# Optimization experiments

Hardware: AMD Instinct MI355X
Metric: run time of the kernel (lower is better)

The kernel has to match this reference:

```python
import jax, jax.numpy as jnp
import numpy as np

B, N_C, N_T, D, DF = 16, 2048, 1024, 2, 2
K, E_OBS = 16, 4
H, DH = 4, 16
F = H * DH  # 64-dim node features (embed_all output)


def setup_inputs() -> dict:
    key = jax.random.key(0)
    ks = jax.random.split(key, 16)
    r = lambda i, shape: jax.random.normal(ks[i], shape, jnp.float32) * 0.05
    d_in = E_OBS + D + DF  # obs(4) + s(2) + f(2) = 8
    return dict(
        s_ctx=jax.random.normal(ks[0], (B, N_C, D), jnp.float32),
        f_ctx=jax.random.normal(ks[1], (B, N_C, DF), jnp.float32),
        s_test=jax.random.normal(ks[2], (B, N_T, D), jnp.float32),
        emb_obs=r(3, (2, E_OBS)),
        W1=r(4, (d_in, 256)), b1=jnp.zeros((256,), jnp.float32),
        W2=r(5, (256, 128)), b2=jnp.zeros((128,), jnp.float32),
        W3=r(6, (128, F)), b3=jnp.zeros((F,), jnp.float32),
        ln_g=jnp.ones((F,), jnp.float32), ln_b=jnp.zeros((F,), jnp.float32),
        Wg=r(7, (F, F)),
        a_src=r(8, (H, DH)), a_dst=r(9, (H, DH)),
        We=r(10, (D, H)), be=jnp.zeros((H,), jnp.float32),
        H1=r(11, (F, 256)), c1=jnp.zeros((256,), jnp.float32),
        H2=r(12, (256, 64)), c2=jnp.zeros((64,), jnp.float32),
        H3=r(13, (64, 2)), c3=jnp.zeros((2,), jnp.float32),
    )


def _knn(q, ctx, k):
    # q [B,Nq,D], ctx [B,Nc,D] -> neighbor indices [B,Nq,K] and displacement edge feats [B,Nq,K,D]
    d2 = (jnp.sum(q * q, -1)[:, :, None] + jnp.sum(ctx * ctx, -1)[:, None, :]
          - 2.0 * jnp.einsum('bqd,bcd->bqc', q, ctx))
    _, idx = jax.lax.top_k(-d2, k)
    nb = jax.vmap(lambda c, i: c[i])(ctx, idx)  # gather neighbor coords per batch
    return idx, q[:, :, None, :] - nb


def _mlp3(x, W1, b1, W2, b2, W3, b3):
    x = jax.nn.gelu(x @ W1 + b1)
    x = jax.nn.gelu(x @ W2 + b2)
    return x @ W3 + b3


def _ln(x, g, b):
    mu = jnp.mean(x, -1, keepdims=True)
    v = jnp.var(x, -1, keepdims=True)
    return (x - mu) * jax.lax.rsqrt(v + 1e-6) * g + b


def reference(s_ctx, f_ctx, s_test, emb_obs, W1, b1, W2, b2, W3, b3, ln_g, ln_b,
              Wg, a_src, a_dst, We, be, H1, c1, H2, c2, H3, c3):
    # --- build kNN graph (ctx->ctx and ctx->test edges, K per receiver) ---
    s_cc, d_cc = _knn(s_ctx, s_ctx, K)
    s_ct, d_ct = _knn(s_test, s_ctx, K)
    edges = jnp.concatenate([d_cc.reshape(-1, D), d_ct.reshape(-1, D)], axis=0)  # [E, D]
    off = (jnp.arange(B) * N_C)[:, None, None]
    senders = jnp.concatenate([(s_cc + off).reshape(-1), (s_ct + off).reshape(-1)])  # [E]
    # receivers == repeat(arange(N), K): edges are grouped K-per-node in node order.

    # --- node embedding: [obs_embed | s | f] -> MLP -> LayerNorm ---
    ctx_in = jnp.concatenate([jnp.broadcast_to(emb_obs[1], (B, N_C, E_OBS)), s_ctx, f_ctx], -1)
    test_in = jnp.concatenate([jnp.broadcast_to(emb_obs[0], (B, N_T, E_OBS)), s_test,
                               jnp.zeros((B, N_T, DF), s_test.dtype)], -1)
    n_ctx = _ln(_mlp3(ctx_in, W1, b1, W2, b2, W3, b3), ln_g, ln_b)
    n_test = _ln(_mlp3(test_in, W1, b1, W2, b2, W3, b3), ln_g, ln_b)
    nodes = jnp.concatenate([n_ctx.reshape(B * N_C, F), n_test.reshape(B * N_T, F)], 0)
    N = B * (N_C + N_T)

    # --- edge-biased GAT message passing (K incoming edges per node) ---
    xp = (nodes @ Wg).reshape(N, H, DH)
    msg = xp[senders].reshape(N, K, H, DH)  # gather sender features
    sc = (jnp.einsum('nkhd,hd->nkh', msg, a_src)
          + jnp.einsum('nhd,hd->nh', xp, a_dst)[:, None, :])
    sc = jax.nn.leaky_relu(sc, 0.2) + (edges @ We + be).reshape(N, K, H)  # edge bias
    alpha = jax.nn.softmax(sc, axis=1)  # softmax over the K neighbors
    out = jnp.einsum('nkh,nkhd->nhd', alpha, msg).reshape(N, F)
    nodes = nodes + out  # residual

    # --- head on test nodes + diagonal MVN output ---
    n_t = nodes[-B * N_T:].reshape(B, N_T, F)
    o = jax.nn.gelu(n_t @ H1 + c1)
    o = jax.nn.gelu(o @ H2 + c2)
    o = o @ H3 + c3  # [B, N_t, 2]
    mean = o[..., 0:1]
    scale = jax.nn.softplus(o[..., 1:2])
    return jnp.concatenate([mean, scale], -1)
```

## Files before the change

kernel.cpp:

```cpp
#include <hip/hip_runtime.h>
#include <math.h>

#define NB 16
#define NCTX 2048
#define NTEST 1024
#define NCTX_TOT (NB*NCTX)
#define NTEST_TOT (NB*NTEST)
#define NTOT (NCTX_TOT + NTEST_TOT)

typedef _Float16 half8 __attribute__((ext_vector_type(8)));
typedef _Float16 half4 __attribute__((ext_vector_type(4)));
typedef float f32x4 __attribute__((ext_vector_type(4)));

__device__ __forceinline__ float gelu_f(float x) {
  float x3 = x * x * x;
  float y = 0.7978845608028654f * fmaf(0.044715f, x3, x);
  float e = __expf(2.0f * y);
  float th = 1.0f - 2.0f * __builtin_amdgcn_rcpf(e + 1.0f);
  return 0.5f * x * (1.0f + th);
}

__device__ __forceinline__ void fma4(float4& a, float s, float4 w) {
  a.x = fmaf(s, w.x, a.x);
  a.y = fmaf(s, w.y, a.y);
  a.z = fmaf(s, w.z, a.z);
  a.w = fmaf(s, w.w, a.w);
}

__device__ __forceinline__ float4 ldg4(const float* p) {
  return *reinterpret_cast<const float4*>(p);
}

__device__ __forceinline__ unsigned fkey(float f) {
  unsigned u = __float_as_uint(f);
  return (u & 0x80000000u) ? ~u : (u ^ 0x80000000u);
}
__device__ __forceinline__ float unfkey(unsigned k) {
  return (k & 0x80000000u) ? __uint_as_float(k ^ 0x80000000u)
                           : __uint_as_float(~k);
}

__global__ __launch_bounds__(256, 6) void knn_prep_kernel(
    const float* __restrict__ s_ctx, const float* __restrict__ s_test,
    int* __restrict__ senders,
    const float* __restrict__ W1, const float* __restrict__ b1,
    const float* __restrict__ emb,
    const float* __restrict__ W2, const float* __restrict__ W3,
    const float* __restrict__ Wg,
    const float* __restrict__ H1, const float* __restrict__ H2,
    _Float16* __restrict__ W2P, _Float16* __restrict__ W3P,
    _Float16* __restrict__ WgP,
    _Float16* __restrict__ H1P, _Float16* __restrict__ H2P,
    float* __restrict__ ctype)
{
  __shared__ __align__(16) unsigned long long sk[4][128];
  const int blk = blockIdx.x;

  if (blk < 40) {
    const int t = blk*256 + (int)threadIdx.x;
    if (t < 4096) {
      int i = t;
      int j = i >> 9, ks = (i >> 6) & 7, l = i & 63;
      int col = 16*j + (l & 15);
      int k0  = ks*32 + (l >> 4)*8;
      half8 o;
      #pragma unroll
      for (int e = 0; e < 8; ++e) o[e] = (_Float16)W2[(k0 + e)*128 + col];
      *reinterpret_cast<half8*>(&W2P[(size_t)i*8]) = o;
    } else if (t < 5120) {
      int i = t - 4096;
      int j = i >> 8, ks = (i >> 6) & 3, l = i & 63;
      int col = 16*j + (l & 15);
      int k0  = ks*32 + (l >> 4)*8;
      half8 o;
      #pragma unroll
      for (int e = 0; e < 8; ++e) o[e] = (_Float16)W3[(k0 + e)*64 + col];
      *reinterpret_cast<half8*>(&W3P[(size_t)i*8]) = o;
    } else if (t < 5632) {
      int i = t - 5120;
      int j = i >> 7, ks = (i >> 6) & 1, l = i & 63;
      int col = 16*j + (l & 15);
      int k0  = ks*32 + (l >> 4)*8;
      half8 o;
      #pragma unroll
      for (int e = 0; e < 8; ++e) o[e] = (_Float16)Wg[(k0 + e)*64 + col];
      *reinterpret_cast<half8*>(&WgP[(size_t)i*8]) = o;
    } else if (t < 7680) {
      int i = t - 5632;
      int j = i >> 7, ks = (i >> 6) & 1, l = i & 63;
      int col = 16*j + (l & 15);
      int k0  = ks*32 + (l >> 4)*8;
      half8 o;
      #pragma unroll
      for (int e = 0; e < 8; ++e) o[e] = (_Float16)H1[(k0 + e)*256 + col];
      *reinterpret_cast<half8*>(&H1P[(size_t)i*8]) = o;
    } else if (t < 9728) {
      int i = t - 7680;
      int j = i >> 9, ks = (i >> 6) & 7, l = i & 63;
      int col = 16*j + (l & 15);
      int k0  = ks*32 + (l >> 4)*8;
      half8 o;
      #pragma unroll
      for (int e = 0; e < 8; ++e) o[e] = (_Float16)H2[(k0 + e)*64 + col];
      *reinterpret_cast<half8*>(&H2P[(size_t)i*8]) = o;
    } else {
      int i = t - 9728;
      int ty = i >> 8, c = i & 255;
      float acc = b1[c];
      #pragma unroll
      for (int k = 0; k < 4; ++k) acc = fmaf(emb[ty*4 + k], W1[k*256 + c], acc);
      ctype[i] = acc;
    }
    return;
  }

  const int t    = threadIdx.x;
  const int lane = t & 63;
  const int w    = t >> 6;
  const int blk2 = blk - 40;
  const int bb   = blk2 >> 8;
  const int q    = (blk2 & 255) * 4 + w;
  const int trow = bb * NTEST + q;

  const float* cb = s_ctx + (size_t)bb * NCTX * 2;
  const float qx = s_test[(size_t)trow*2];
  const float qy = s_test[(size_t)trow*2 + 1];
  const float qq = __fadd_rn(__fmul_rn(qx,qx), __fmul_rn(qy,qy));

  float d[32];
  float mn = 3.4e38f;
  #pragma unroll
  for (int it = 0; it < 32; ++it) {
    float2 p = *reinterpret_cast<const float2*>(&cb[2*(it*64 + lane)]);
    float ss  = __fadd_rn(__fmul_rn(p.x,p.x), __fmul_rn(p.y,p.y));
    float dot = __fadd_rn(__fmul_rn(qx, p.x), __fmul_rn(qy, p.y));
    float d2  = __fsub_rn(__fadd_rn(qq, ss), __fmul_rn(2.0f, dot));
    d[it] = d2;
    mn = fminf(mn, d2);
  }

  unsigned key = fkey(mn);
  unsigned acc = 0u;
  #pragma unroll
  for (int bit = 31; bit >= 0; --bit) {
    unsigned candv = acc | (1u << bit);
    unsigned long long bal = __ballot(key < candv);
    if (__popcll(bal) < 16) acc = candv;
  }
  const float Tf = unfkey(acc);

  int base = 0;
  #pragma unroll
  for (int it = 0; it < 32; ++it) {
    bool pr = (d[it] <= Tf);
    unsigned long long m = __ballot(pr);
    if (pr) {
      int pos = base + __popcll(m & ((1ULL << lane) - 1ULL));
      if (pos < 128)
        sk[w][pos] = ((unsigned long long)fkey(d[it]) << 32)
                   | (unsigned)(it*64 + lane);
    }
    base += __popcll(m);
  }
  const int S = base;

  if (S <= 32) {
    if (lane >= S && lane < 32) sk[w][lane] = ~0ULL;
    unsigned long long pm = sk[w][lane & 31];
    int r0 = 0;
    #pragma unroll
    for (int j = 0; j < 32; ++j)
      r0 += (int)(sk[w][j] < pm);
    if (lane < S && r0 < 16)
      senders[(size_t)trow*16 + r0] = bb*NCTX + (int)(pm & 0xFFFFFFFFu);
  } else if (S <= 128) {
    unsigned long long p0 = (lane      < S) ? sk[w][lane]      : ~0ULL;
    unsigned long long p1 = (lane + 64 < S) ? sk[w][lane + 64] : ~0ULL;
    int r0 = 0, r1 = 0;
    for (int j = 0; j < S; ++j) {
      unsigned long long kj = sk[w][j];
      r0 += (int)(kj < p0);
      r1 += (int)(kj < p1);
    }
    if (lane < S && r0 < 16)
      senders[(size_t)trow*16 + r0] = bb*NCTX + (int)(p0 & 0xFFFFFFFFu);
    if (lane + 64 < S && r1 < 16)
      senders[(size_t)trow*16 + r1] = bb*NCTX + (int)(p1 & 0xFFFFFFFFu);
  } else {
    if (lane == 0) {
      float dist[16]; int ind[16];
      #pragma unroll
      for (int j=0;j<16;++j){ dist[j]=3.4e38f; ind[j]=0; }
      for (int c = 0; c < NCTX; ++c) {
        float2 p = *reinterpret_cast<const float2*>(&cb[2*c]);
        float ss  = __fadd_rn(__fmul_rn(p.x,p.x), __fmul_rn(p.y,p.y));
        float dot = __fadd_rn(__fmul_rn(qx, p.x), __fmul_rn(qy, p.y));
        float d2  = __fsub_rn(__fadd_rn(qq, ss), __fmul_rn(2.0f, dot));
        if (d2 < dist[15]) {
          float dj = d2; int ij = c;
          #pragma unroll
          for (int j = 0; j < 16; ++j) {
            bool sw = dj < dist[j];
            float td = dist[j]; int ti = ind[j];
            dist[j] = sw ? dj : td;  ind[j] = sw ? ij : ti;
            dj = sw ? td : dj;       ij = sw ? ti : ij;
          }
        }
      }
      for (int j = 0; j < 16; ++j)
        senders[(size_t)trow*16 + j] = bb*NCTX + ind[j];
    }
  }
}

__global__ __launch_bounds__(256, 4) void mlp_kernel(
    const float* __restrict__ s_ctx, const float* __restrict__ f_ctx,
    const float* __restrict__ s_test,
    const float* __restrict__ ctype, const float* __restrict__ W1,
    const _Float16* __restrict__ W2P, const float* __restrict__ b2,
    const _Float16* __restrict__ W3P, const float* __restrict__ b3,
    const float* __restrict__ ln_g, const float* __restrict__ ln_b,
    const _Float16* __restrict__ WgP,
    const float* __restrict__ a_src, const float* __restrict__ a_dst,
    float* __restrict__ nodes, _Float16* __restrict__ xph,
    float* __restrict__ xps, float* __restrict__ xpd)
{
  __shared__ __align__(16) char smem[34816];
  const int t    = threadIdx.x;
  const int lane = t & 63;
  const int w    = t >> 6;
  const int id   = blockIdx.x;
  char* slice = smem + w * 8704;
  _Float16* h1t  = reinterpret_cast<_Float16*>(slice);
  float (*xin)[4] = reinterpret_cast<float(*)[4]>(slice + 8448);
  _Float16* h2   = h1t;
  _Float16* nodh = h1t + 16*136;
  const int cn = lane & 15;
  const int kg = lane >> 4;
  const int m0 = (id*4 + w) * 16;
  const bool is_ctx = (m0 < NCTX_TOT);

  const _Float16* bQ2 = W2P + lane*8;
  const _Float16* bQ3 = W3P + lane*8;
  const _Float16* bQg = WgP + lane*8;

  half8 bb2[8];
  #pragma unroll
  for (int j = 0; j < 8; ++j)
    bb2[j] = *reinterpret_cast<const half8*>(bQ2 + j*4096);

  {
    int r = lane >> 2, c = lane & 3;
    int n = m0 + r;
    float v;
    if (is_ctx) v = (c < 2) ? s_ctx[2*(size_t)n + c] : f_ctx[2*(size_t)n + (c-2)];
    else { int tn = n - NCTX_TOT; v = (c < 2) ? s_test[2*(size_t)tn + c] : 0.f; }
    xin[r][c] = v;
  }

  {
    const int c0 = lane * 4;
    float4 w4 = ldg4(&W1[4*256 + c0]);
    float4 w5 = ldg4(&W1[5*256 + c0]);
    float4 w6 = ldg4(&W1[6*256 + c0]);
    float4 w7 = ldg4(&W1[7*256 + c0]);
    float4 cbv = ldg4(&ctype[(is_ctx ? 256 : 0) + c0]);
    #pragma unroll
    for (int r = 0; r < 16; ++r) {
      float4 xi = *reinterpret_cast<const float4*>(&xin[r][0]);
      float4 a = cbv;
      fma4(a, xi.x, w4); fma4(a, xi.y, w5);
      fma4(a, xi.z, w6); fma4(a, xi.w, w7);
      half4 o = { (_Float16)gelu_f(a.x), (_Float16)gelu_f(a.y),
                  (_Float16)gelu_f(a.z), (_Float16)gelu_f(a.w) };
      *reinterpret_cast<half4*>(&h1t[r*264 + c0]) = o;
    }
  }

  {
    f32x4 acc[8];
    #pragma unroll
    for (int j = 0; j < 8; ++j) {
      float bv = b2[16*j + cn];
      acc[j] = (f32x4){bv, bv, bv, bv};
    }
    const _Float16* aP = h1t + cn*264 + kg*8;
    #pragma unroll
    for (int ks = 0; ks < 8; ++ks) {
      half8 a = *reinterpret_cast<const half8*>(aP + ks*32);
      half8 bn[8];
      if (ks < 7) {
        #pragma unroll
        for (int j = 0; j < 8; ++j)
          bn[j] = *reinterpret_cast<const half8*>(bQ2 + j*4096 + (ks+1)*512);
      }
      #pragma unroll
      for (int j = 0; j < 8; ++j)
        acc[j] = __builtin_amdgcn_mfma_f32_16x16x32_f16(a, bb2[j], acc[j], 0, 0, 0);
      if (ks < 7) {
        #pragma unroll
        for (int j = 0; j < 8; ++j) bb2[j] = bn[j];
      }
    }
    #pragma unroll
    for (int j = 0; j < 8; ++j)
      #pragma unroll
      for (int r = 0; r < 4; ++r) {
        int m = kg*4 + r;
        h2[m*136 + 16*j + cn] = (_Float16)gelu_f(acc[j][r]);
      }
  }

  {
    f32x4 acc[4];
    #pragma unroll
    for (int j = 0; j < 4; ++j) {
      float bv = b3[16*j + cn];
      acc[j] = (f32x4){bv, bv, bv, bv};
    }
    const _Float16* aP = h2 + cn*136 + kg*8;
    half8 bb[4];
    #pragma unroll
    for (int j = 0; j < 4; ++j)
      bb[j] = *reinterpret_cast<const half8*>(bQ3 + j*2048);
    #pragma unroll
    for (int ks = 0; ks < 4; ++ks) {
      half8 a = *reinterpret_cast<const half8*>(aP + ks*32);
      half8 bn[4];
      if (ks < 3) {
        #pragma unroll
        for (int j = 0; j < 4; ++j)
          bn[j] = *reinterpret_cast<const half8*>(bQ3 + j*2048 + (ks+1)*512);
      }
      #pragma unroll
      for (int j = 0; j < 4; ++j)
        acc[j] = __builtin_amdgcn_mfma_f32_16x16x32_f16(a, bb[j], acc[j], 0, 0, 0);
      if (ks < 3) {
        #pragma unroll
        for (int j = 0; j < 4; ++j) bb[j] = bn[j];
      }
    }
    float gv[4], bvv[4];
    #pragma unroll
    for (int j = 0; j < 4; ++j) { gv[j] = ln_g[16*j+cn]; bvv[j] = ln_b[16*j+cn]; }
    const bool is_test = !is_ctx;
    #pragma unroll
    for (int r = 0; r < 4; ++r) {
      float sv = 0.f, sq = 0.f;
      #pragma unroll
      for (int j = 0; j < 4; ++j) {
        float v = acc[j][r];
        sv += v; sq += v*v;
      }
      #pragma unroll
      for (int o = 1; o < 16; o <<= 1) {
        sv += __shfl_xor(sv, o);
        sq += __shfl_xor(sq, o);
      }
      float mean = sv * (1.0f/64.0f);
      float var  = sq * (1.0f/64.0f) - mean*mean;
      float rstd = rsqrtf(var + 1e-6f);
      int m = kg*4 + r;
      #pragma unroll
      for (int j = 0; j < 4; ++j) {
        float v = (acc[j][r] - mean) * rstd * gv[j] + bvv[j];
        nodh[m*72 + 16*j + cn] = (_Float16)v;
        if (is_test)
          nodes[(size_t)(m0 + m)*64 + 16*j + cn] = v;
      }
    }
  }

  {
    f32x4 acc[4];
    #pragma unroll
    for (int j = 0; j < 4; ++j) acc[j] = (f32x4){0.f, 0.f, 0.f, 0.f};
    const _Float16* aP = nodh + cn*72 + kg*8;
    half8 bg0[4], bg1[4];
    #pragma unroll
    for (int j = 0; j < 4; ++j) {
      bg0[j] = *reinterpret_cast<const half8*>(bQg + j*1024);
      bg1[j] = *reinterpret_cast<const half8*>(bQg + j*1024 + 512);
    }
    half8 a0 = *reinterpret_cast<const half8*>(aP);
    half8 a1 = *reinterpret_cast<const half8*>(aP + 32);
    #pragma unroll
    for (int j = 0; j < 4; ++j)
      acc[j] = __builtin_amdgcn_mfma_f32_16x16x32_f16(a0, bg0[j], acc[j], 0, 0, 0);
    #pragma unroll
    for (int j = 0; j < 4; ++j)
      acc[j] = __builtin_amdgcn_mfma_f32_16x16x32_f16(a1, bg1[j], acc[j], 0, 0, 0);
    #pragma unroll
    for (int r = 0; r < 4; ++r) {
      int m = kg*4 + r;
      #pragma unroll
      for (int j = 0; j < 4; ++j)
        xph[(size_t)(m0 + m)*64 + 16*j + cn] = (_Float16)acc[j][r];
    }
    const float* av = is_ctx ? a_src : a_dst;
    float av0 = av[cn], av1 = av[16+cn], av2 = av[32+cn], av3 = av[48+cn];
    #pragma unroll
    for (int r = 0; r < 4; ++r) {
      float p0 = acc[0][r]*av0, p1 = acc[1][r]*av1;
      float p2 = acc[2][r]*av2, p3 = acc[3][r]*av3;
      #pragma unroll
      for (int o = 1; o < 16; o <<= 1) {
        p0 += __shfl_xor(p0, o); p1 += __shfl_xor(p1, o);
        p2 += __shfl_xor(p2, o); p3 += __shfl_xor(p3, o);
      }
      if (cn == 0) {
        int m = kg*4 + r;
        float4 v = make_float4(p0, p1, p2, p3);
        if (is_ctx)
          *reinterpret_cast<float4*>(&xps[(size_t)(m0 + m)*4]) = v;
        else
          *reinterpret_cast<float4*>(&xpd[(size_t)(m0 + m - NCTX_TOT)*4]) = v;
      }
    }
  }
}

__global__ __launch_bounds__(64, 3) void back_kernel(
    const float* __restrict__ s_ctx, const float* __restrict__ s_test,
    const _Float16* __restrict__ xph, const int* __restrict__ senders,
    const float* __restrict__ xps, const float* __restrict__ xpd,
    const float* __restrict__ We, const float* __restrict__ be,
    const float* __restrict__ nodes,
    const _Float16* __restrict__ H1P, const float* __restrict__ c1,
    const _Float16* __restrict__ H2P, const float* __restrict__ c2,
    const float* __restrict__ H3, const float* __restrict__ c3,
    float* __restrict__ outp)
{
  __shared__ __align__(16) _Float16 xinh[16*72];
  __shared__ __align__(16) _Float16 h1[16*264];
  const int lane = threadIdx.x;
  const int cn   = lane & 15;
  const int kg   = lane >> 4;
  const int bid  = blockIdx.x;
  const int L    = (bid & 7)*256 + (bid >> 3);
  const int row0 = L * 8;

  #pragma unroll
  for (int rr = 8; rr < 16; ++rr) xinh[rr*72 + lane] = (_Float16)0.f;

  {
    const int h  = kg;
    const int kk = cn;
    const int hb = lane & 48;
    const float we0 = We[h], we1 = We[4+h], beh = be[h];
    for (int rr = 0; rr < 8; ++rr) {
      const int trow = row0 + rr;
      int s = senders[(size_t)trow*16 + kk];
      s = (s < 0) ? 0 : ((s >= NCTX_TOT) ? NCTX_TOT - 1 : s);
      float pre = xps[(size_t)s*4 + h] + xpd[(size_t)trow*4 + h];
      float lr  = pre >= 0.f ? pre : 0.2f * pre;
      const float qx = s_test[(size_t)trow*2];
      const float qy = s_test[(size_t)trow*2 + 1];
      float ex = qx - s_ctx[(size_t)s*2];
      float ey = qy - s_ctx[(size_t)s*2 + 1];
      float sc = lr + fmaf(ex, we0, fmaf(ey, we1, beh));
      float mx = sc;
      #pragma unroll
      for (int o = 1; o < 16; o <<= 1) mx = fmaxf(mx, __shfl_xor(mx, o));
      float e = __expf(sc - mx);
      float sum = e;
      #pragma unroll
      for (int o = 1; o < 16; o <<= 1) sum += __shfl_xor(sum, o);
      float alpha = e / sum;
      float outv = 0.f;
      #pragma unroll
      for (int k = 0; k < 16; ++k) {
        int   sk = __shfl(s, k);
        float al = __shfl(alpha, hb + k);
        outv = fmaf(al, (float)xph[(size_t)sk*64 + lane], outv);
      }
      float xv = nodes[(size_t)(NCTX_TOT + trow)*64 + lane] + outv;
      xinh[rr*72 + lane] = (_Float16)xv;
    }
  }

  {
    const _Float16* aP  = xinh + cn*72 + kg*8;
    const _Float16* bQ1 = H1P + lane*8;
    half8 a0 = *reinterpret_cast<const half8*>(aP);
    half8 a1 = *reinterpret_cast<const half8*>(aP + 32);
    #pragma unroll
    for (int g = 0; g < 2; ++g) {
      f32x4 acc[8];
      #pragma unroll
      for (int j = 0; j < 8; ++j) {
        float bv = c1[16*(g*8 + j) + cn];
        acc[j] = (f32x4){bv, bv, bv, bv};
      }
      half8 b0[8], b1[8];
      #pragma unroll
      for (int j = 0; j < 8; ++j) {
        b0[j] = *reinterpret_cast<const half8*>(bQ1 + ((g*8 + j)*2 + 0)*512);
        b1[j] = *reinterpret_cast<const half8*>(bQ1 + ((g*8 + j)*2 + 1)*512);
      }
      #pragma unroll
      for (int j = 0; j < 8; ++j)
        acc[j] = __builtin_amdgcn_mfma_f32_16x16x32_f16(a0, b0[j], acc[j], 0, 0, 0);
      #pragma unroll
      for (int j = 0; j < 8; ++j)
        acc[j] = __builtin_amdgcn_mfma_f32_16x16x32_f16(a1, b1[j], acc[j], 0, 0, 0);
      #pragma unroll
      for (int j = 0; j < 8; ++j)
        #pragma unroll
        for (int r = 0; r < 4; ++r)
          h1[(kg*4 + r)*264 + 16*(g*8 + j) + cn] = (_Float16)gelu_f(acc[j][r]);
    }
  }

  {
    f32x4 acc[4];
    #pragma unroll
    for (int j = 0; j < 4; ++j) {
      float bv = c2[16*j + cn];
      acc[j] = (f32x4){bv, bv, bv, bv};
    }
    const _Float16* aP  = h1 + cn*264 + kg*8;
    const _Float16* bQ2 = H2P + lane*8;
    half8 bb[4];
    #pragma unroll
    for (int j = 0; j < 4; ++j)
      bb[j] = *reinterpret_cast<const half8*>(bQ2 + j*4096);
    #pragma unroll
    for (int ks = 0; ks < 8; ++ks) {
      half8 a = *reinterpret_cast<const half8*>(aP + ks*32);
      half8 bn[4];
      if (ks < 7) {
        #pragma unroll
        for (int j = 0; j < 4; ++j)
          bn[j] = *reinterpret_cast<const half8*>(bQ2 + j*4096 + (ks+1)*512);
      }
      #pragma unroll
      for (int j = 0; j < 4; ++j)
        acc[j] = __builtin_amdgcn_mfma_f32_16x16x32_f16(a, bb[j], acc[j], 0, 0, 0);
      if (ks < 7) {
        #pragma unroll
        for (int j = 0; j < 4; ++j) bb[j] = bn[j];
      }
    }
    float h30[4], h31[4];
    #pragma unroll
    for (int j = 0; j < 4; ++j) {
      h30[j] = H3[(16*j + cn)*2 + 0];
      h31[j] = H3[(16*j + cn)*2 + 1];
    }
    const float c30 = c3[0], c31 = c3[1];
    #pragma unroll
    for (int r = 0; r < 4; ++r) {
      float p0 = 0.f, p1 = 0.f;
      #pragma unroll
      for (int j = 0; j < 4; ++j) {
        float g = gelu_f(acc[j][r]);
        p0 = fmaf(g, h30[j], p0);
        p1 = fmaf(g, h31[j], p1);
      }
      #pragma unroll
      for (int o = 1; o < 16; o <<= 1) {
        p0 += __shfl_xor(p0, o);
        p1 += __shfl_xor(p1, o);
      }
      if (cn == 0 && kg < 2) {
        int row = row0 + kg*4 + r;
        float m = p0 + c30;
        float sa = p1 + c31;
        float sv = fmaxf(sa, 0.f) + log1pf(__expf(-fabsf(sa)));
        outp[(size_t)row*2 + 0] = m;
        outp[(size_t)row*2 + 1] = sv;
      }
    }
  }
}

extern "C" void kernel_launch(void* const* d_in, const int* in_sizes, int n_in,
                              void* d_out, int out_size, void* d_ws, size_t ws_size,
                              hipStream_t stream) {
  const float* s_ctx  = (const float*)d_in[0];
  const float* f_ctx  = (const float*)d_in[1];
  const float* s_test = (const float*)d_in[2];
  const float* emb    = (const float*)d_in[3];
  const float* W1 = (const float*)d_in[4];
  const float* b1 = (const float*)d_in[5];
  const float* W2 = (const float*)d_in[6];
  const float* b2 = (const float*)d_in[7];
  const float* W3 = (const float*)d_in[8];
  const float* b3 = (const float*)d_in[9];
  const float* ln_g = (const float*)d_in[10];
  const float* ln_b = (const float*)d_in[11];
  const float* Wg = (const float*)d_in[12];
  const float* a_src = (const float*)d_in[13];
  const float* a_dst = (const float*)d_in[14];
  const float* We = (const float*)d_in[15];
  const float* be = (const float*)d_in[16];
  const float* H1 = (const float*)d_in[17];
  const float* c1 = (const float*)d_in[18];
  const float* H2 = (const float*)d_in[19];
  const float* c2 = (const float*)d_in[20];
  const float* H3 = (const float*)d_in[21];
  const float* c3 = (const float*)d_in[22];

  float* nodes   = (float*)d_ws;
  _Float16* xph  = (_Float16*)(nodes + (size_t)NTOT*64);
  int*   senders = (int*)(xph + (size_t)NTOT*64);
  _Float16* W2P  = (_Float16*)(senders + (size_t)NTEST_TOT*16);
  _Float16* W3P  = W2P + 32768;
  _Float16* WgP  = W3P + 8192;
  _Float16* H1P  = WgP + 4096;
  _Float16* H2P  = H1P + 16384;
  float*   ctype = (float*)(H2P + 16384);
  float*   xps   = ctype + 512;
  float*   xpd   = xps + (size_t)NCTX_TOT*4;
  float* outp    = (float*)d_out;

  hipLaunchKernelGGL(knn_prep_kernel, dim3(4136), dim3(256), 0, stream,
                     s_ctx, s_test, senders,
                     W1, b1, emb, W2, W3, Wg, H1, H2,
                     W2P, W3P, WgP, H1P, H2P, ctype);
  hipLaunchKernelGGL(mlp_kernel, dim3(768), dim3(256), 0, stream,
                     s_ctx, f_ctx, s_test, ctype, W1,
                     W2P, b2, W3P, b3, ln_g, ln_b, WgP,
                     a_src, a_dst, nodes, xph, xps, xpd);
  hipLaunchKernelGGL(back_kernel, dim3(2048), dim3(64), 0, stream,
                     s_ctx, s_test, xph, senders, xps, xpd, We, be,
                     nodes, H1P, c1, H2P, c2, H3, c3, outp);
}
```

Baseline: 71.71 us.

## Process two kNN queries per wavefront using half-wave lanes

The kNN selection in knn_prep_kernel now assigns two test queries to each 64-lane wavefront, each handled by 32 lanes that scan 64 context points apiece. The radix-select threshold search and the ballot-based compaction run both halves at once by splitting ballot masks, which halves the grid size and the number of ballot/bit-search iterations per query. In exchange each lane keeps twice as many distances in registers (the launch-bounds occupancy hint is lowered to match), and the rank-sort fallback loops to the larger of the two halves' candidate counts.

```diff
diff --git a/kernel.cpp b/kernel.cpp
--- a/kernel.cpp
+++ b/kernel.cpp
@@ -40,7 +40,7 @@
                            : __uint_as_float(~k);
 }
 
-__global__ __launch_bounds__(256, 6) void knn_prep_kernel(
+__global__ __launch_bounds__(256, 4) void knn_prep_kernel(
     const float* __restrict__ s_ctx, const float* __restrict__ s_test,
     int* __restrict__ senders,
     const float* __restrict__ W1, const float* __restrict__ b1,
@@ -53,7 +53,7 @@
     _Float16* __restrict__ H1P, _Float16* __restrict__ H2P,
     float* __restrict__ ctype)
 {
-  __shared__ __align__(16) unsigned long long sk[4][128];
+  __shared__ __align__(16) unsigned long long sk[4][2][128];
   const int blk = blockIdx.x;
 
   if (blk < 40) {
@@ -117,9 +117,12 @@
   const int t    = threadIdx.x;
   const int lane = t & 63;
   const int w    = t >> 6;
+  const int half = lane >> 5;
+  const int hl   = lane & 31;
   const int blk2 = blk - 40;
-  const int bb   = blk2 >> 8;
-  const int q    = (blk2 & 255) * 4 + w;
+  const int qid  = blk2*8 + (w << 1) + half;
+  const int bb   = qid >> 10;
+  const int q    = qid & 1023;
   const int trow = bb * NTEST + q;
 
   const float* cb = s_ctx + (size_t)bb * NCTX * 2;
@@ -127,11 +130,11 @@
   const float qy = s_test[(size_t)trow*2 + 1];
   const float qq = __fadd_rn(__fmul_rn(qx,qx), __fmul_rn(qy,qy));
 
-  float d[32];
+  float d[64];
   float mn = 3.4e38f;
   #pragma unroll
-  for (int it = 0; it < 32; ++it) {
-    float2 p = *reinterpret_cast<const float2*>(&cb[2*(it*64 + lane)]);
+  for (int it = 0; it < 64; ++it) {
+    float2 p = *reinterpret_cast<const float2*>(&cb[2*(it*32 + hl)]);
     float ss  = __fadd_rn(__fmul_rn(p.x,p.x), __fmul_rn(p.y,p.y));
     float dot = __fadd_rn(__fmul_rn(qx, p.x), __fmul_rn(qy, p.y));
     float d2  = __fsub_rn(__fadd_rn(qq, ss), __fmul_rn(2.0f, dot));
@@ -140,54 +143,72 @@
   }
 
   unsigned key = fkey(mn);
-  unsigned acc = 0u;
+  unsigned accA = 0u, accB = 0u;
   #pragma unroll
   for (int bit = 31; bit >= 0; --bit) {
-    unsigned candv = acc | (1u << bit);
-    unsigned long long bal = __ballot(key < candv);
-    if (__popcll(bal) < 16) acc = candv;
-  }
-  const float Tf = unfkey(acc);
-
-  int base = 0;
+    unsigned cA = accA | (1u << bit);
+    unsigned cB = accB | (1u << bit);
+    unsigned cand = half ? cB : cA;
+    unsigned long long bal = __ballot(key < cand);
+    int pA = __popcll(bal & 0xFFFFFFFFull);
+    int pB = __popcll(bal >> 32);
+    if (pA < 16) accA = cA;
+    if (pB < 16) accB = cB;
+  }
+  const float Tf = unfkey(half ? accB : accA);
+
+  int baseA = 0, baseB = 0;
   #pragma unroll
-  for (int it = 0; it < 32; ++it) {
+  for (int it = 0; it < 64; ++it) {
     bool pr = (d[it] <= Tf);
     unsigned long long m = __ballot(pr);
+    int mb   = __popcll(m & ((1ULL << lane) - 1ULL));
+    int pLow = __popcll(m & 0xFFFFFFFFull);
     if (pr) {
-      int pos = base + __popcll(m & ((1ULL << lane) - 1ULL));
+      int pos = half ? (baseB + mb - pLow) : (baseA + mb);
       if (pos < 128)
-        sk[w][pos] = ((unsigned long long)fkey(d[it]) << 32)
-                   | (unsigned)(it*64 + lane);
-    }
-    base += __popcll(m);
-  }
-  const int S = base;
-
-  if (S <= 32) {
-    if (lane >= S && lane < 32) sk[w][lane] = ~0ULL;
-    unsigned long long pm = sk[w][lane & 31];
+        sk[w][half][pos] = ((unsigned long long)fkey(d[it]) << 32)
+                         | (unsigned)(it*32 + hl);
+    }
+    baseA += pLow;
+    baseB += __popcll(m >> 32);
+  }
+  const int SA = baseA, SB = baseB;
+  const int Sh = half ? SB : SA;
+
+  if (SA <= 32 && SB <= 32) {
+    if (hl >= Sh) sk[w][half][hl] = ~0ULL;
+    unsigned long long pm = sk[w][half][hl];
     int r0 = 0;
     #pragma unroll
     for (int j = 0; j < 32; ++j)
-      r0 += (int)(sk[w][j] < pm);
-    if (lane < S && r0 < 16)
+      r0 += (int)(sk[w][half][j] < pm);
+    if (hl < Sh && r0 < 16)
       senders[(size_t)trow*16 + r0] = bb*NCTX + (int)(pm & 0xFFFFFFFFu);
-  } else if (S <= 128) {
-    unsigned long long p0 = (lane      < S) ? sk[w][lane]      : ~0ULL;
-    unsigned long long p1 = (lane + 64 < S) ? sk[w][lane + 64] : ~0ULL;
-    int r0 = 0, r1 = 0;
-    for (int j = 0; j < S; ++j) {
-      unsigned long long kj = sk[w][j];
+  } else if (SA <= 128 && SB <= 128) {
+    unsigned long long p0 = (hl      < Sh) ? sk[w][half][hl]      : ~0ULL;
+    unsigned long long p1 = (hl + 32 < Sh) ? sk[w][half][hl + 32] : ~0ULL;
+    unsigned long long p2 = (hl + 64 < Sh) ? sk[w][half][hl + 64] : ~0ULL;
+    unsigned long long p3 = (hl + 96 < Sh) ? sk[w][half][hl + 96] : ~0ULL;
+    int r0 = 0, r1 = 0, r2 = 0, r3 = 0;
+    const int mx = (SA > SB) ? SA : SB;
+    for (int j = 0; j < mx; ++j) {
+      unsigned long long kj = (j < Sh) ? sk[w][half][j] : ~0ULL;
       r0 += (int)(kj < p0);
       r1 += (int)(kj < p1);
-    }
-    if (lane < S && r0 < 16)
+      r2 += (int)(kj < p2);
+      r3 += (int)(kj < p3);
+    }
+    if (hl      < Sh && r0 < 16)
       senders[(size_t)trow*16 + r0] = bb*NCTX + (int)(p0 & 0xFFFFFFFFu);
-    if (lane + 64 < S && r1 < 16)
+    if (hl + 32 < Sh && r1 < 16)
       senders[(size_t)trow*16 + r1] = bb*NCTX + (int)(p1 & 0xFFFFFFFFu);
+    if (hl + 64 < Sh && r2 < 16)
+      senders[(size_t)trow*16 + r2] = bb*NCTX + (int)(p2 & 0xFFFFFFFFu);
+    if (hl + 96 < Sh && r3 < 16)
+      senders[(size_t)trow*16 + r3] = bb*NCTX + (int)(p3 & 0xFFFFFFFFu);
   } else {
-    if (lane == 0) {
+    if (hl == 0) {
       float dist[16]; int ind[16];
       #pragma unroll
       for (int j=0;j<16;++j){ dist[j]=3.4e38f; ind[j]=0; }
@@ -615,7 +636,7 @@
   float*   xpd   = xps + (size_t)NCTX_TOT*4;
   float* outp    = (float*)d_out;
 
-  hipLaunchKernelGGL(knn_prep_kernel, dim3(4136), dim3(256), 0, stream,
+  hipLaunchKernelGGL(knn_prep_kernel, dim3(2088), dim3(256), 0, stream,
                      s_ctx, s_test, senders,
                      W1, b1, emb, W2, W3, Wg, H1, H2,
                      W2P, W3P, WgP, H1P, H2P, ctype);
```

After: 79.41 us. +10.7%, slower.
